# Performance work log

Hardware: AMD Instinct MI355X
Metric: run time of the kernel (lower is better)

Reference implementation:

```python
import jax, jax.numpy as jnp
import numpy as np

NUM_HEADS = 8
MAX_REL = 32  # max_relative_positions
LN_EPS = 1e-5


def _conv1x1(x, W, b):
    # x: (B, C, H, W), W: (Cout, Cin), b: (Cout,)
    return jnp.einsum('bchw,oc->bohw', x, W) + b[None, :, None, None]


def setup_inputs() -> dict:
    key = jax.random.key(0)
    ks = jax.random.split(key, 10)
    B, C, H, W = 2, 512, 48, 48
    L = H * W
    s = 1.0 / np.sqrt(C)
    inp = {
        'x': jax.random.normal(ks[0], (B, C, H, W), jnp.float32),
        'mask': jax.random.randint(ks[1], (1, NUM_HEADS, L, L), 0, 2).astype(bool),
        'learnable_pos': jax.random.normal(ks[2], (1, C, H, W), jnp.float32) * 0.02,
        'Wq': jax.random.normal(ks[3], (C, C), jnp.float32) * s,
        'bq': jnp.zeros((C,), jnp.float32),
        'Wk': jax.random.normal(ks[4], (C, C), jnp.float32) * s,
        'bk': jnp.zeros((C,), jnp.float32),
        'Wv': jax.random.normal(ks[5], (C, C), jnp.float32) * s,
        'bv': jnp.zeros((C,), jnp.float32),
        'Wo': jax.random.normal(ks[6], (C, C), jnp.float32) * s,
        'bo': jnp.zeros((C,), jnp.float32),
        'rel_table': jax.random.normal(ks[7], (NUM_HEADS, 2 * MAX_REL + 1), jnp.float32) * 0.02,
        'ln_gamma': jnp.ones((C,), jnp.float32),
        'ln_beta': jnp.zeros((C,), jnp.float32),
    }
    return inp


def reference(x, mask, learnable_pos, Wq, bq, Wk, bk, Wv, bv, Wo, bo,
              rel_table, ln_gamma, ln_beta):
    B, C, H, W = x.shape
    L = H * W
    hd = C // NUM_HEADS
    residual = x

    xp = x + learnable_pos
    q = _conv1x1(xp, Wq, bq)
    k = _conv1x1(xp, Wk, bk)
    v = _conv1x1(xp, Wv, bv)

    def split_heads(t):  # (B,C,H,W) -> (B, heads, L, hd)
        return t.reshape(B, NUM_HEADS, hd, L).transpose(0, 1, 3, 2)

    q, k, v = split_heads(q), split_heads(k), split_heads(v)

    scale = 1.0 / np.sqrt(hd).astype(np.float32)
    scores = jnp.einsum('bhld,bhmd->bhlm', q, k) * scale  # (B,H,L,L)

    # relative positional bias per head
    pos = jnp.arange(L)
    rp = jnp.clip(pos[:, None] - pos[None, :], -MAX_REL, MAX_REL) + MAX_REL  # (L,L)
    scores = scores + rel_table[:, rp][None]  # (1,heads,L,L) broadcast

    scores = jnp.where(mask, scores, jnp.float32(-1e9))
    attn = jax.nn.softmax(scores, axis=-1)

    out = jnp.einsum('bhlm,bhmd->bhld', attn, v)  # (B,heads,L,hd)
    out = out.transpose(0, 1, 3, 2).reshape(B, C, H, W)
    out = _conv1x1(out, Wo, bo)

    y = residual + out
    # LayerNorm over channels (channels-last permute in original)
    yl = y.transpose(0, 2, 3, 1)  # (B,H,W,C)
    mu = jnp.mean(yl, axis=-1, keepdims=True)
    var = jnp.var(yl, axis=-1, keepdims=True)
    yl = (yl - mu) * jax.lax.rsqrt(var + LN_EPS) * ln_gamma + ln_beta
    return yl.transpose(0, 3, 1, 2)
```

## Files before the change

### kernel.cpp

```cpp
#include <hip/hip_runtime.h>
#include <cstdint>

#define L_SEQ 2304
#define CDIM  512
#define NHEADS 8
#define HD    64
#define LL    ((size_t)L_SEQ * L_SEQ)
#define ROWS_TOT (16 * L_SEQ)
#define PERBL ((size_t)2 * L_SEQ * 512)

typedef short  s8v  __attribute__((ext_vector_type(8)));
typedef float  f4v  __attribute__((ext_vector_type(4)));

__device__ __forceinline__ ushort f2bf(float f) {
    union { float f; uint32_t u; } v; v.f = f;
    uint32_t u = v.u;
    uint32_t r = (u + 0x7FFFu + ((u >> 16) & 1u)) >> 16;
    return (ushort)r;
}

__device__ __forceinline__ float bf2f(ushort u) {
    union { uint32_t u; float f; } v; v.u = (uint32_t)u << 16;
    return v.f;
}

__global__ __launch_bounds__(256) void prep_w(
    const float* __restrict__ Wq, const float* __restrict__ Wk,
    const float* __restrict__ Wv, const float* __restrict__ Wo,
    ushort* __restrict__ wb)
{
    const int i   = blockIdx.x * 256 + threadIdx.x;
    const int mat = i >> 16;
    const int j   = i & 65535;
    const float* src = (mat == 0) ? Wq : (mat == 1) ? Wk : (mat == 2) ? Wv : Wo;
    const float4 w = ((const float4*)src)[j];
    ushort4 o;
    o.x = f2bf(w.x); o.y = f2bf(w.y); o.z = f2bf(w.z); o.w = f2bf(w.w);
    ((ushort4*)(wb + (size_t)mat * 262144))[j] = o;
}

__global__ __launch_bounds__(256) void xpose(
    const float* __restrict__ x, const float* __restrict__ pos,
    ushort* __restrict__ xt)
{
    __shared__ ushort T[64][72];
    const int l0 = blockIdx.x * 64;
    const int c0 = blockIdx.y * 64;
    const int b  = blockIdx.z;
    const int t  = threadIdx.x;
    const int cc = t >> 2;
    const int l4 = (t & 3) * 16;
    const size_t off  = ((size_t)b * CDIM + c0 + cc) * L_SEQ + l0 + l4;
    const size_t poff = (size_t)(c0 + cc) * L_SEQ + l0 + l4;
    #pragma unroll
    for (int j4 = 0; j4 < 4; j4++) {
        const float4 xv = *(const float4*)&x[off + j4 * 4];
        const float4 pv = *(const float4*)&pos[poff + j4 * 4];
        T[cc][l4 + j4 * 4 + 0] = f2bf(xv.x + pv.x);
        T[cc][l4 + j4 * 4 + 1] = f2bf(xv.y + pv.y);
        T[cc][l4 + j4 * 4 + 2] = f2bf(xv.z + pv.z);
        T[cc][l4 + j4 * 4 + 3] = f2bf(xv.w + pv.w);
    }
    __syncthreads();
    const int lr = t >> 2;
    const int c4 = (t & 3) * 16;
    ushort o[16];
    #pragma unroll
    for (int j = 0; j < 16; j++) o[j] = T[c4 + j][lr];
    ushort* dst = &xt[((size_t)b * L_SEQ + l0 + lr) * 512 + c0 + c4];
    *(ushort4*)&dst[0]  = *(ushort4*)&o[0];
    *(ushort4*)&dst[4]  = *(ushort4*)&o[4];
    *(ushort4*)&dst[8]  = *(ushort4*)&o[8];
    *(ushort4*)&dst[12] = *(ushort4*)&o[12];
}

__global__ __launch_bounds__(256) void qkv_mfma(
    const ushort* __restrict__ xt, const ushort* __restrict__ wb,
    const float* __restrict__ bq, const float* __restrict__ bk,
    const float* __restrict__ bv,
    ushort* __restrict__ q_t, ushort* __restrict__ k_t, ushort* __restrict__ v_t)
{
    const int l0  = blockIdx.x * 64;
    const int o0  = blockIdx.y * 64;
    const int b   = blockIdx.z / 3;
    const int mat = blockIdx.z % 3;
    const int t = threadIdx.x, w = t >> 6, lane = t & 63;
    const int n16 = lane & 15, q4 = lane >> 4;

    const ushort* A = xt + ((size_t)b * L_SEQ + l0 + w * 16 + n16) * 512 + q4 * 8;
    const ushort* B = wb + (size_t)mat * 262144 + (size_t)(o0 + n16) * 512 + q4 * 8;

    f4v acc[4] = {{0.f,0.f,0.f,0.f},{0.f,0.f,0.f,0.f},{0.f,0.f,0.f,0.f},{0.f,0.f,0.f,0.f}};
    #pragma unroll
    for (int kc = 0; kc < 512; kc += 32) {
        const s8v a = *(const s8v*)&A[kc];
        #pragma unroll
        for (int t4 = 0; t4 < 4; t4++) {
            const s8v bf = *(const s8v*)&B[(size_t)(t4 * 16) * 512 + kc];
            acc[t4] = __builtin_amdgcn_mfma_f32_16x16x32_bf16(a, bf, acc[t4], 0, 0, 0);
        }
    }

    const float* bias = (mat == 0) ? bq : (mat == 1) ? bk : bv;
    const int h = o0 >> 6;
    const int rowbase = l0 + w * 16 + q4 * 4;

    if (mat < 2) {
        const float sc = (mat == 0) ? 0.125f : 1.0f;
        ushort* op = (mat == 0 ? q_t : k_t) + ((size_t)(b * NHEADS + h)) * L_SEQ * HD;
        #pragma unroll
        for (int t4 = 0; t4 < 4; t4++) {
            const float bi = bias[o0 + t4 * 16 + n16];
            #pragma unroll
            for (int r = 0; r < 4; r++)
                op[(size_t)(rowbase + r) * HD + t4 * 16 + n16] = f2bf((acc[t4][r] + bi) * sc);
        }
    } else {
        ushort* op = v_t + ((size_t)(b * NHEADS + h)) * HD * L_SEQ;
        #pragma unroll
        for (int t4 = 0; t4 < 4; t4++) {
            const float bi = bias[o0 + t4 * 16 + n16];
            ushort4 st;
            st.x = f2bf(acc[t4][0] + bi);
            st.y = f2bf(acc[t4][1] + bi);
            st.z = f2bf(acc[t4][2] + bi);
            st.w = f2bf(acc[t4][3] + bi);
            *(ushort4*)&op[(size_t)(t4 * 16 + n16) * L_SEQ + rowbase] = st;
        }
    }
}

__global__ __launch_bounds__(256) void flash_attn_mfma(
    const ushort* __restrict__ q, const ushort* __restrict__ k,
    const ushort* __restrict__ vt, const int* __restrict__ mask,
    const float* __restrict__ rel_table, ushort* __restrict__ Opart,
    float* __restrict__ Mpart, float* __restrict__ Lpart)
{
    __shared__ __align__(16) ushort Kf[512 * 8];
    __shared__ __align__(16) ushort Vf[512 * 8];
    __shared__ __align__(16) ushort Pb[4 * 16 * 72];
    __shared__ float rt[65];

    const int t    = threadIdx.x;
    const int id   = blockIdx.x;
    const int h    = id & 7;
    const int s2   = id >> 3;
    const int b    = s2 & 1;
    const int half = (s2 >> 1) & 1;
    const int qb   = s2 >> 2;
    const int bh   = b * NHEADS + h;
    const int l0   = qb * 64;
    const int w    = t >> 6;
    const int lane = t & 63;
    const int n16  = lane & 15;
    const int q4   = lane >> 4;

    if (t < 65) rt[t] = rel_table[h * 65 + t];

    const ushort* qp = q  + (size_t)bh * L_SEQ * HD;
    const ushort* kp = k  + (size_t)bh * L_SEQ * HD;
    const ushort* vp = vt + (size_t)bh * HD * L_SEQ;
    const int*    mp = mask + (size_t)h * LL;

    const int qrow = l0 + w * 16 + n16;
    const s8v qA0 = *(const s8v*)&qp[(size_t)qrow * HD + q4 * 8];
    const s8v qA1 = *(const s8v*)&qp[(size_t)qrow * HD + 32 + q4 * 8];

    f4v O[4] = {{0.f,0.f,0.f,0.f},{0.f,0.f,0.f,0.f},{0.f,0.f,0.f,0.f},{0.f,0.f,0.f,0.f}};
    float mrun[4] = {-3e38f, -3e38f, -3e38f, -3e38f};
    float lrun[4] = {0.f, 0.f, 0.f, 0.f};

    int sT[2], sS[2], sQ[2], sN[2];
    #pragma unroll
    for (int cc = 0; cc < 2; cc++) {
        const int c = t + cc * 256;
        const int g = c >> 6;
        sT[cc] = g >> 1; sS[cc] = g & 1;
        sQ[cc] = (c >> 4) & 3; sN[cc] = c & 15;
    }

    const int rowbase = l0 + w * 16 + q4 * 4;
    const int kbase = half * 1152;

    for (int mt = 0; mt < 18; mt++) {
        const int mb = kbase + mt * 64;
        __syncthreads();
        #pragma unroll
        for (int cc = 0; cc < 2; cc++) {
            const int c = t + cc * 256;
            const int key = sT[cc] * 16 + sN[cc];
            const int d0  = sS[cc] * 32 + sQ[cc] * 8;
            *(s8v*)&Kf[c * 8] = *(const s8v*)&kp[(size_t)(mb + key) * HD + d0];
            const int dd = sT[cc] * 16 + sN[cc];
            *(s8v*)&Vf[c * 8] = *(const s8v*)&vp[(size_t)dd * L_SEQ + mb + d0];
        }
        __syncthreads();

        int mreg[4][4];
        #pragma unroll
        for (int t4 = 0; t4 < 4; t4++)
            #pragma unroll
            for (int r = 0; r < 4; r++)
                mreg[t4][r] = mp[(size_t)(rowbase + r) * L_SEQ + mb + t4 * 16 + n16];

        f4v S[4];
        #pragma unroll
        for (int t4 = 0; t4 < 4; t4++) {
            const s8v b0 = *(const s8v*)&Kf[((t4 * 2 + 0) * 64 + lane) * 8];
            const s8v b1 = *(const s8v*)&Kf[((t4 * 2 + 1) * 64 + lane) * 8];
            f4v acc = {0.f, 0.f, 0.f, 0.f};
            acc = __builtin_amdgcn_mfma_f32_16x16x32_bf16(qA0, b0, acc, 0, 0, 0);
            acc = __builtin_amdgcn_mfma_f32_16x16x32_bf16(qA1, b1, acc, 0, 0, 0);
            S[t4] = acc;
        }

        #pragma unroll
        for (int t4 = 0; t4 < 4; t4++) {
            const int A = (l0 + w * 16) - (mb + t4 * 16);
            if (A >= 47) {
                const float bu = rt[64];
                #pragma unroll
                for (int r = 0; r < 4; r++) S[t4][r] += bu;
            } else if (A <= -47) {
                const float bu = rt[0];
                #pragma unroll
                for (int r = 0; r < 4; r++) S[t4][r] += bu;
            } else {
                #pragma unroll
                for (int r = 0; r < 4; r++) {
                    int dix = A + q4 * 4 + r - n16;
                    dix = min(max(dix, -32), 32) + 32;
                    S[t4][r] += rt[dix];
                }
            }
            #pragma unroll
            for (int r = 0; r < 4; r++)
                if (mreg[t4][r] == 0) S[t4][r] = -1e9f;
        }

        float mx[4];
        #pragma unroll
        for (int r = 0; r < 4; r++) {
            float m0 = fmaxf(fmaxf(S[0][r], S[1][r]), fmaxf(S[2][r], S[3][r]));
            m0 = fmaxf(m0, __shfl_xor(m0, 1));
            m0 = fmaxf(m0, __shfl_xor(m0, 2));
            m0 = fmaxf(m0, __shfl_xor(m0, 4));
            m0 = fmaxf(m0, __shfl_xor(m0, 8));
            mx[r] = m0;
        }
        float al[4];
        #pragma unroll
        for (int r = 0; r < 4; r++) {
            const float mn = fmaxf(mrun[r], mx[r]);
            al[r] = __expf(mrun[r] - mn);
            mrun[r] = mn;
            float sum = 0.f;
            #pragma unroll
            for (int t4 = 0; t4 < 4; t4++) {
                const float p = __expf(S[t4][r] - mn);
                S[t4][r] = p;
                sum += p;
                Pb[w * 1152 + (q4 * 4 + r) * 72 + t4 * 16 + n16] = f2bf(p);
            }
            sum += __shfl_xor(sum, 1);
            sum += __shfl_xor(sum, 2);
            sum += __shfl_xor(sum, 4);
            sum += __shfl_xor(sum, 8);
            lrun[r] = lrun[r] * al[r] + sum;
        }

        const s8v pf0 = *(const s8v*)&Pb[w * 1152 + n16 * 72 + q4 * 8];
        const s8v pf1 = *(const s8v*)&Pb[w * 1152 + n16 * 72 + 32 + q4 * 8];
        #pragma unroll
        for (int t4 = 0; t4 < 4; t4++) {
            f4v o = O[t4];
            #pragma unroll
            for (int r = 0; r < 4; r++) o[r] *= al[r];
            const s8v v0 = *(const s8v*)&Vf[((t4 * 2 + 0) * 64 + lane) * 8];
            const s8v v1 = *(const s8v*)&Vf[((t4 * 2 + 1) * 64 + lane) * 8];
            o = __builtin_amdgcn_mfma_f32_16x16x32_bf16(pf0, v0, o, 0, 0, 0);
            o = __builtin_amdgcn_mfma_f32_16x16x32_bf16(pf1, v1, o, 0, 0, 0);
            O[t4] = o;
        }
    }

    ushort* op = Opart + (size_t)half * PERBL + (size_t)b * L_SEQ * 512;
    #pragma unroll
    for (int r = 0; r < 4; r++) {
        const size_t base = (size_t)(rowbase + r) * 512 + h * 64;
        #pragma unroll
        for (int t4 = 0; t4 < 4; t4++)
            op[base + t4 * 16 + n16] = f2bf(O[t4][r]);
    }
    if (n16 == 0) {
        const size_t sb = (size_t)half * ROWS_TOT + (size_t)bh * L_SEQ;
        #pragma unroll
        for (int r = 0; r < 4; r++) {
            Mpart[sb + rowbase + r] = mrun[r];
            Lpart[sb + rowbase + r] = lrun[r];
        }
    }
}

__global__ __launch_bounds__(256) void combine_kernel(
    const ushort* __restrict__ O01, const float* __restrict__ Mp,
    const float* __restrict__ Lp, ushort* __restrict__ at)
{
    const int i   = blockIdx.x * 256 + threadIdx.x;
    const int c8  = i & 63;
    const int row = i >> 6;
    const int b   = row / L_SEQ;
    const int l   = row - b * L_SEQ;
    const int h   = c8 >> 3;
    const size_t s = (size_t)(b * NHEADS + h) * L_SEQ + l;
    const float m0 = Mp[s], m1 = Mp[ROWS_TOT + s];
    const float l0 = Lp[s], l1 = Lp[ROWS_TOT + s];
    const float M  = fmaxf(m0, m1);
    const float w0 = __expf(m0 - M);
    const float w1 = __expf(m1 - M);
    const float inv = 1.0f / (l0 * w0 + l1 * w1);
    const float f0 = w0 * inv;
    const float f1 = w1 * inv;
    const size_t o = (size_t)row * 512 + c8 * 8;
    const ushort4 a0 = *(const ushort4*)&O01[o];
    const ushort4 a1 = *(const ushort4*)&O01[o + 4];
    const ushort4 c0 = *(const ushort4*)&O01[PERBL + o];
    const ushort4 c1 = *(const ushort4*)&O01[PERBL + o + 4];
    ushort4 r0, r1;
    r0.x = f2bf(bf2f(a0.x) * f0 + bf2f(c0.x) * f1);
    r0.y = f2bf(bf2f(a0.y) * f0 + bf2f(c0.y) * f1);
    r0.z = f2bf(bf2f(a0.z) * f0 + bf2f(c0.z) * f1);
    r0.w = f2bf(bf2f(a0.w) * f0 + bf2f(c0.w) * f1);
    r1.x = f2bf(bf2f(a1.x) * f0 + bf2f(c1.x) * f1);
    r1.y = f2bf(bf2f(a1.y) * f0 + bf2f(c1.y) * f1);
    r1.z = f2bf(bf2f(a1.z) * f0 + bf2f(c1.z) * f1);
    r1.w = f2bf(bf2f(a1.w) * f0 + bf2f(c1.w) * f1);
    *(ushort4*)&at[o]     = r0;
    *(ushort4*)&at[o + 4] = r1;
}

__global__ __launch_bounds__(256) void out_mfma(
    const ushort* __restrict__ at, const ushort* __restrict__ wb,
    const float* __restrict__ bo, const float* __restrict__ x,
    float* __restrict__ y)
{
    const int l0 = blockIdx.x * 64;
    const int o0 = blockIdx.y * 64;
    const int b  = blockIdx.z;
    const int t = threadIdx.x, w = t >> 6, lane = t & 63;
    const int n16 = lane & 15, q4 = lane >> 4;

    const ushort* A = at + ((size_t)b * L_SEQ + l0 + w * 16 + n16) * 512 + q4 * 8;
    const ushort* B = wb + (size_t)3 * 262144 + (size_t)(o0 + n16) * 512 + q4 * 8;

    f4v acc[4] = {{0.f,0.f,0.f,0.f},{0.f,0.f,0.f,0.f},{0.f,0.f,0.f,0.f},{0.f,0.f,0.f,0.f}};
    #pragma unroll
    for (int kc = 0; kc < 512; kc += 32) {
        const s8v a = *(const s8v*)&A[kc];
        #pragma unroll
        for (int t4 = 0; t4 < 4; t4++) {
            const s8v bf = *(const s8v*)&B[(size_t)(t4 * 16) * 512 + kc];
            acc[t4] = __builtin_amdgcn_mfma_f32_16x16x32_bf16(a, bf, acc[t4], 0, 0, 0);
        }
    }

    const int rowbase = l0 + w * 16 + q4 * 4;
    #pragma unroll
    for (int t4 = 0; t4 < 4; t4++) {
        const int o = o0 + t4 * 16 + n16;
        const float bi = bo[o];
        const size_t off = ((size_t)b * CDIM + o) * L_SEQ + rowbase;
        const float4 xv = *(const float4*)&x[off];
        float4 st;
        st.x = acc[t4][0] + bi + xv.x;
        st.y = acc[t4][1] + bi + xv.y;
        st.z = acc[t4][2] + bi + xv.z;
        st.w = acc[t4][3] + bi + xv.w;
        *(float4*)&y[off] = st;
    }
}

__global__ __launch_bounds__(256) void ln_kernel(
    float* __restrict__ y, const float* __restrict__ gamma,
    const float* __restrict__ beta)
{
    const int t  = threadIdx.x;
    const int pi = t & 63;
    const int g  = t >> 6;
    const int pos = blockIdx.x * 64 + pi;
    const int b = (pos >= L_SEQ) ? 1 : 0;
    const int l = pos - b * L_SEQ;
    float* col = y + (size_t)b * CDIM * L_SEQ + l;

    float s = 0.f, sq = 0.f;
    for (int c = g * 128; c < g * 128 + 128; c++) {
        const float v = col[(size_t)c * L_SEQ];
        s += v; sq += v * v;
    }
    __shared__ float S1[4][64];
    __shared__ float S2[4][64];
    S1[g][pi] = s; S2[g][pi] = sq;
    __syncthreads();
    if (g == 0) {
        s  = S1[0][pi] + S1[1][pi] + S1[2][pi] + S1[3][pi];
        sq = S2[0][pi] + S2[1][pi] + S2[2][pi] + S2[3][pi];
        const float mu = s * (1.0f / CDIM);
        const float var = sq * (1.0f / CDIM) - mu * mu;
        S1[0][pi] = mu;
        S2[0][pi] = rsqrtf(var + 1e-5f);
    }
    __syncthreads();
    const float mu = S1[0][pi];
    const float rs = S2[0][pi];
    for (int c = g * 128; c < g * 128 + 128; c++) {
        const float v = col[(size_t)c * L_SEQ];
        col[(size_t)c * L_SEQ] = (v - mu) * rs * gamma[c] + beta[c];
    }
}

extern "C" void kernel_launch(void* const* d_in, const int* in_sizes, int n_in,
                              void* d_out, int out_size, void* d_ws, size_t ws_size,
                              hipStream_t stream) {
    const float* x    = (const float*)d_in[0];
    const int* mask   = (const int*)d_in[1];
    const float* pos  = (const float*)d_in[2];
    const float* Wq   = (const float*)d_in[3];
    const float* bq   = (const float*)d_in[4];
    const float* Wk   = (const float*)d_in[5];
    const float* bk   = (const float*)d_in[6];
    const float* Wv   = (const float*)d_in[7];
    const float* bv   = (const float*)d_in[8];
    const float* Wo   = (const float*)d_in[9];
    const float* bo   = (const float*)d_in[10];
    const float* rel  = (const float*)d_in[11];
    const float* gam  = (const float*)d_in[12];
    const float* bet  = (const float*)d_in[13];

    ushort* qw  = (ushort*)d_ws;
    ushort* kw  = qw + PERBL;
    ushort* vw  = kw + PERBL;
    ushort* xtw = vw + PERBL;
    ushort* wbw = xtw + PERBL;
    ushort* Opart = wbw + (size_t)4 * 512 * 512;
    float* Mpart = (float*)(Opart + 2 * PERBL);
    float* Lpart = Mpart + 2 * ROWS_TOT;
    ushort* attnT = xtw;
    float* y = (float*)d_out;

    prep_w<<<dim3(1024), 256, 0, stream>>>(Wq, Wk, Wv, Wo, wbw);

    xpose<<<dim3(L_SEQ / 64, CDIM / 64, 2), 256, 0, stream>>>(x, pos, xtw);

    qkv_mfma<<<dim3(L_SEQ / 64, CDIM / 64, 6), 256, 0, stream>>>(
        xtw, wbw, bq, bk, bv, qw, kw, vw);

    flash_attn_mfma<<<dim3(1152), 256, 0, stream>>>(qw, kw, vw, mask, rel,
                                                    Opart, Mpart, Lpart);

    combine_kernel<<<dim3(1152), 256, 0, stream>>>(Opart, Mpart, Lpart, attnT);

    out_mfma<<<dim3(L_SEQ / 64, CDIM / 64, 2), 256, 0, stream>>>(
        attnT, wbw, bo, x, y);

    ln_kernel<<<(2 * L_SEQ) / 64, 256, 0, stream>>>(y, gam, bet);
}
```

Before: 453.5 us.

## Stage weight tiles in shared memory for projection GEMMs and widen LayerNorm grid

```diff
diff --git a/kernel.cpp b/kernel.cpp
--- a/kernel.cpp
+++ b/kernel.cpp
@@ -80,6 +80,7 @@
     const float* __restrict__ bv,
     ushort* __restrict__ q_t, ushort* __restrict__ k_t, ushort* __restrict__ v_t)
 {
+    __shared__ __align__(16) ushort Bs[1024 * 8];
     const int l0  = blockIdx.x * 64;
     const int o0  = blockIdx.y * 64;
     const int b   = blockIdx.z / 3;
@@ -88,16 +89,34 @@
     const int n16 = lane & 15, q4 = lane >> 4;
 
     const ushort* A = xt + ((size_t)b * L_SEQ + l0 + w * 16 + n16) * 512 + q4 * 8;
-    const ushort* B = wb + (size_t)mat * 262144 + (size_t)(o0 + n16) * 512 + q4 * 8;
+    const ushort* W = wb + (size_t)mat * 262144;
+
+    int sRow[4], sCol[4];
+    #pragma unroll
+    for (int i = 0; i < 4; i++) {
+        const int c  = t + 256 * i;
+        const int fr = c >> 6, ln = c & 63;
+        sRow[i] = o0 + (fr & 3) * 16 + (ln & 15);
+        sCol[i] = (fr >> 2) * 32 + (ln >> 4) * 8;
+    }
 
     f4v acc[4] = {{0.f,0.f,0.f,0.f},{0.f,0.f,0.f,0.f},{0.f,0.f,0.f,0.f},{0.f,0.f,0.f,0.f}};
-    #pragma unroll
-    for (int kc = 0; kc < 512; kc += 32) {
-        const s8v a = *(const s8v*)&A[kc];
-        #pragma unroll
-        for (int t4 = 0; t4 < 4; t4++) {
-            const s8v bf = *(const s8v*)&B[(size_t)(t4 * 16) * 512 + kc];
-            acc[t4] = __builtin_amdgcn_mfma_f32_16x16x32_bf16(a, bf, acc[t4], 0, 0, 0);
+    for (int kb = 0; kb < 512; kb += 128) {
+        __syncthreads();
+        #pragma unroll
+        for (int i = 0; i < 4; i++) {
+            const int c = t + 256 * i;
+            *(s8v*)&Bs[c * 8] = *(const s8v*)&W[(size_t)sRow[i] * 512 + kb + sCol[i]];
+        }
+        __syncthreads();
+        #pragma unroll
+        for (int ks = 0; ks < 4; ks++) {
+            const s8v a = *(const s8v*)&A[kb + ks * 32];
+            #pragma unroll
+            for (int t4 = 0; t4 < 4; t4++) {
+                const s8v bf = *(const s8v*)&Bs[((ks * 4 + t4) * 64 + lane) * 8];
+                acc[t4] = __builtin_amdgcn_mfma_f32_16x16x32_bf16(a, bf, acc[t4], 0, 0, 0);
+            }
         }
     }
 
@@ -344,6 +363,7 @@
     const float* __restrict__ bo, const float* __restrict__ x,
     float* __restrict__ y)
 {
+    __shared__ __align__(16) ushort Bs[1024 * 8];
     const int l0 = blockIdx.x * 64;
     const int o0 = blockIdx.y * 64;
     const int b  = blockIdx.z;
@@ -351,16 +371,34 @@
     const int n16 = lane & 15, q4 = lane >> 4;
 
     const ushort* A = at + ((size_t)b * L_SEQ + l0 + w * 16 + n16) * 512 + q4 * 8;
-    const ushort* B = wb + (size_t)3 * 262144 + (size_t)(o0 + n16) * 512 + q4 * 8;
+    const ushort* W = wb + (size_t)3 * 262144;
+
+    int sRow[4], sCol[4];
+    #pragma unroll
+    for (int i = 0; i < 4; i++) {
+        const int c  = t + 256 * i;
+        const int fr = c >> 6, ln = c & 63;
+        sRow[i] = o0 + (fr & 3) * 16 + (ln & 15);
+        sCol[i] = (fr >> 2) * 32 + (ln >> 4) * 8;
+    }
 
     f4v acc[4] = {{0.f,0.f,0.f,0.f},{0.f,0.f,0.f,0.f},{0.f,0.f,0.f,0.f},{0.f,0.f,0.f,0.f}};
-    #pragma unroll
-    for (int kc = 0; kc < 512; kc += 32) {
-        const s8v a = *(const s8v*)&A[kc];
-        #pragma unroll
-        for (int t4 = 0; t4 < 4; t4++) {
-            const s8v bf = *(const s8v*)&B[(size_t)(t4 * 16) * 512 + kc];
-            acc[t4] = __builtin_amdgcn_mfma_f32_16x16x32_bf16(a, bf, acc[t4], 0, 0, 0);
+    for (int kb = 0; kb < 512; kb += 128) {
+        __syncthreads();
+        #pragma unroll
+        for (int i = 0; i < 4; i++) {
+            const int c = t + 256 * i;
+            *(s8v*)&Bs[c * 8] = *(const s8v*)&W[(size_t)sRow[i] * 512 + kb + sCol[i]];
+        }
+        __syncthreads();
+        #pragma unroll
+        for (int ks = 0; ks < 4; ks++) {
+            const s8v a = *(const s8v*)&A[kb + ks * 32];
+            #pragma unroll
+            for (int t4 = 0; t4 < 4; t4++) {
+                const s8v bf = *(const s8v*)&Bs[((ks * 4 + t4) * 64 + lane) * 8];
+                acc[t4] = __builtin_amdgcn_mfma_f32_16x16x32_bf16(a, bf, acc[t4], 0, 0, 0);
+            }
         }
     }
 
@@ -384,35 +422,36 @@
     float* __restrict__ y, const float* __restrict__ gamma,
     const float* __restrict__ beta)
 {
-    const int t  = threadIdx.x;
-    const int pi = t & 63;
-    const int g  = t >> 6;
-    const int pos = blockIdx.x * 64 + pi;
+    const int t = threadIdx.x;
+    const int p = t & 15;
+    const int g = t >> 4;
+    const int pos = blockIdx.x * 16 + p;
     const int b = (pos >= L_SEQ) ? 1 : 0;
     const int l = pos - b * L_SEQ;
     float* col = y + (size_t)b * CDIM * L_SEQ + l;
 
     float s = 0.f, sq = 0.f;
-    for (int c = g * 128; c < g * 128 + 128; c++) {
+    for (int c = g * 32; c < g * 32 + 32; c++) {
         const float v = col[(size_t)c * L_SEQ];
         s += v; sq += v * v;
     }
-    __shared__ float S1[4][64];
-    __shared__ float S2[4][64];
-    S1[g][pi] = s; S2[g][pi] = sq;
+    __shared__ float S1[16][16];
+    __shared__ float S2[16][16];
+    S1[g][p] = s; S2[g][p] = sq;
     __syncthreads();
-    if (g == 0) {
-        s  = S1[0][pi] + S1[1][pi] + S1[2][pi] + S1[3][pi];
-        sq = S2[0][pi] + S2[1][pi] + S2[2][pi] + S2[3][pi];
-        const float mu = s * (1.0f / CDIM);
-        const float var = sq * (1.0f / CDIM) - mu * mu;
-        S1[0][pi] = mu;
-        S2[0][pi] = rsqrtf(var + 1e-5f);
+    if (t < 16) {
+        float ss = 0.f, qq = 0.f;
+        #pragma unroll
+        for (int gg = 0; gg < 16; gg++) { ss += S1[gg][t]; qq += S2[gg][t]; }
+        const float mu = ss * (1.0f / CDIM);
+        const float var = qq * (1.0f / CDIM) - mu * mu;
+        S1[0][t] = mu;
+        S2[0][t] = rsqrtf(var + 1e-5f);
     }
     __syncthreads();
-    const float mu = S1[0][pi];
-    const float rs = S2[0][pi];
-    for (int c = g * 128; c < g * 128 + 128; c++) {
+    const float mu = S1[0][p];
+    const float rs = S2[0][p];
+    for (int c = g * 32; c < g * 32 + 32; c++) {
         const float v = col[(size_t)c * L_SEQ];
         col[(size_t)c * L_SEQ] = (v - mu) * rs * gamma[c] + beta[c];
     }
@@ -462,5 +501,5 @@
     out_mfma<<<dim3(L_SEQ / 64, CDIM / 64, 2), 256, 0, stream>>>(
         attnT, wbw, bo, x, y);
 
-    ln_kernel<<<(2 * L_SEQ) / 64, 256, 0, stream>>>(y, gam, bet);
-}
+    ln_kernel<<<(2 * L_SEQ) / 16, 256, 0, stream>>>(y, gam, bet);
+}
```

New measurement: 396.2 us. 12.6% less time.
